# Optimization experiments

Measured on AMD Instinct MI355X. Metric: run time of the kernel, lower is better.

The kernel has to match this reference:

```python
import jax, jax.numpy as jnp
import numpy as np

TAU = 1.0
EPS = 1e-5


def _gcn_sparse(x, src, dst, ew, W, b, n):
    # PyG GCNConv: add self-loops (weight 1), sym-normalize, aggregate src->dst
    deg = jax.ops.segment_sum(ew, dst, num_segments=n) + 1.0
    dinv = jnp.where(deg > 0, jax.lax.rsqrt(deg), 0.0)
    h = x @ W
    coef = dinv[src] * ew * dinv[dst]              # [E]
    out = jax.ops.segment_sum(h[src] * coef[:, None], dst, num_segments=n)
    out = out + h * (dinv * dinv)[:, None]         # self-loop term
    return out + b


def _gcn_dense(x, A, W, b):
    # x: [B,N,d], A: [B,N,N] with A[b,i,j] = weight of edge j->i
    n = A.shape[-1]
    Ah = A + jnp.eye(n, dtype=A.dtype)
    deg = Ah.sum(-1)
    dinv = jnp.where(deg > 0, jax.lax.rsqrt(deg), 0.0)
    An = dinv[:, :, None] * Ah * dinv[:, None, :]
    return jnp.einsum('bij,bjd->bid', An, x @ W) + b


def _bn_silu(x, g, be, axes):
    # BatchNorm over node axis (training-mode batch stats, biased var) + SiLU
    m = x.mean(axes, keepdims=True)
    v = x.var(axes, keepdims=True)
    return jax.nn.silu(g * (x - m) * jax.lax.rsqrt(v + EPS) + be)


def setup_inputs() -> dict:
    key = jax.random.key(0)
    ks = jax.random.split(key, 12)
    B, NPG, EPER = 32, 1024, 16384
    CIN, C, K1, K2, OUT = 64, 128, 128, 32, 10
    N, E = B * NPG, B * EPER
    ei = jax.random.randint(ks[0], (2, E), 0, NPG, dtype=jnp.int32)
    off = jnp.repeat(jnp.arange(B, dtype=jnp.int32) * NPG, EPER)
    edge_index = ei + off[None, :]
    x = jax.random.normal(ks[1], (N, CIN), jnp.float32)
    batch = jnp.repeat(jnp.arange(B, dtype=jnp.int32), NPG)
    batch_ptr = jnp.arange(B + 1, dtype=jnp.int32) * NPG
    p = lambda k, s: jax.random.normal(k, s, jnp.float32) * 0.05
    return dict(
        x=x, edge_index=edge_index, batch=batch, batch_ptr=batch_ptr,
        w1a=p(ks[2], (CIN, C)), b1a=jnp.zeros((C,)), g1a=jnp.ones((C,)), be1a=jnp.zeros((C,)),
        w1b=p(ks[3], (C, C)), b1b=jnp.zeros((C,)), g1b=jnp.ones((C,)), be1b=jnp.zeros((C,)),
        wp1=p(ks[4], (C, K1)), bp1=jnp.zeros((K1,)),
        w2a=p(ks[5], (C, C)), b2a=jnp.zeros((C,)), g2a=jnp.ones((C,)), be2a=jnp.zeros((C,)),
        w2b=p(ks[6], (C, C)), b2b=jnp.zeros((C,)), g2b=jnp.ones((C,)), be2b=jnp.zeros((C,)),
        wp2=p(ks[7], (C, K2)), bp2=jnp.zeros((K2,)),
        wl=p(ks[8], (C, OUT)), bl=jnp.zeros((OUT,)))


def reference(x, edge_index, batch, batch_ptr,
              w1a, b1a, g1a, be1a, w1b, b1b, g1b, be1b, wp1, bp1,
              w2a, b2a, g2a, be2a, w2b, b2b, g2b, be2b, wp2, bp2,
              wl, bl):
    n = x.shape[0]
    B = batch_ptr.shape[0] - 1
    npg = n // B                                    # uniform nodes per graph
    src, dst = edge_index[0], edge_index[1]
    ew = jnp.ones((edge_index.shape[1],), x.dtype)  # edge_weight=None -> ones

    # ---- stack 1: sparse GCN residual blocks + stochastic pool ----
    h = _bn_silu(_gcn_sparse(x, src, dst, ew, w1a, b1a, n), g1a, be1a, 0)
    h = h + _bn_silu(_gcn_sparse(h, src, dst, ew, w1b, b1b, n), g1b, be1b, 0)
    s = jax.nn.softmax(_gcn_sparse(h, src, dst, ew, wp1, bp1, n) / TAU, -1)  # [n,K1]
    s3 = s.reshape(B, npg, -1)
    x2 = jnp.einsum('bnc,bnd->bcd', s3, h.reshape(B, npg, -1))   # s^T x  [B,K1,C]
    t = jax.ops.segment_sum(s[src] * ew[:, None], dst, num_segments=n)  # A s
    A2 = jnp.einsum('bnc,bnk->bck', s3, t.reshape(B, npg, -1))   # s^T A s [B,K1,K1]

    # ---- stack 2: dense GCN on pooled graph + stochastic pool ----
    h2 = _bn_silu(_gcn_dense(x2, A2, w2a, b2a), g2a, be2a, (0, 1))
    h2 = h2 + _bn_silu(_gcn_dense(h2, A2, w2b, b2b), g2b, be2b, (0, 1))
    s2 = jax.nn.softmax(_gcn_dense(h2, A2, wp2, bp2) / TAU, -1)  # [B,K1,K2]
    x3 = jnp.einsum('bnc,bnd->bcd', s2, h2)                      # [B,K2,C]

    # global mean pool over nodes per graph, linear, log_softmax
    g = x3.mean(axis=1)
    out = jax.nn.log_softmax(g @ wl + bl, axis=1)
    # aux losses are multiplied by 0 in the original forward -> exact zero
    return (out, jnp.zeros((), x.dtype))
```

## Files before the change

### kernel.cpp

```cpp
#include <hip/hip_runtime.h>
#include <cmath>

#define KSPLIT 8
#define ELL_ST 80

typedef __attribute__((ext_vector_type(8))) short short8;
typedef __attribute__((ext_vector_type(4))) float float4v;

static __device__ __forceinline__ unsigned short f2bf(float f){
  union { float f; unsigned u; } c; c.f = f;
  unsigned r = c.u + 0x7fff + ((c.u >> 16) & 1);
  return (unsigned short)(r >> 16);
}
static __device__ __forceinline__ float u2f(unsigned u){
  union { unsigned u; float f; } c; c.u = u; return c.f;
}
static __device__ __forceinline__ float silu(float y){ return y/(1.f+__expf(-y)); }

static __device__ __forceinline__ void coef_prologue(const float* __restrict__ stats,
                                                     const float* __restrict__ gamma,
                                                     const float* __restrict__ beta,
                                                     float invM, float* lds, int tbase){
  int t = threadIdx.x - tbase;
  if(t >= 0 && t < 128){
    float s = 0.f, q = 0.f;
    #pragma unroll
    for(int k=0;k<8;k++){ s += stats[k*128+t]; q += stats[1024 + k*128+t]; }
    float m = s*invM;
    float v = q*invM - m*m;
    float sc = gamma[t]*rsqrtf(v + 1e-5f);
    lds[t] = sc;
    lds[128+t] = beta[t] - m*sc;
  }
}

__global__ void k_fill_wt(const int* __restrict__ src, const int* __restrict__ dst,
                          int* __restrict__ cursor, int* __restrict__ esrc, int E,
                          const float* __restrict__ w1a, const float* __restrict__ w1b,
                          const float* __restrict__ wp1, unsigned short* __restrict__ t1a,
                          unsigned short* __restrict__ t1b, unsigned short* __restrict__ tp1,
                          int CIN){
  int i = blockIdx.x*256 + threadIdx.x;
  if(i < E){
    int d = dst[i];
    int p = atomicAdd(&cursor[d], 1);
    if(p < ELL_ST) esrc[(size_t)d*ELL_ST + p] = src[i];
  } else {
    int j = i - E;
    int n1 = CIN*128, n2 = 128*128;
    if(j >= 0 && j < n1){
      int k = j >> 7, c = j & 127;
      t1a[(size_t)c*CIN + k] = f2bf(w1a[j]);
    } else if(j >= n1 && j < n1+n2){
      int jj = j - n1; int k = jj >> 7, c = jj & 127;
      t1b[(size_t)c*128 + k] = f2bf(w1b[jj]);
    } else if(j >= n1+n2 && j < n1+2*n2){
      int jj = j - n1 - n2; int k = jj >> 7, c = jj & 127;
      tp1[(size_t)c*128 + k] = f2bf(wp1[jj]);
    }
  }
}

__global__ void k_gemm_mfma(const float* __restrict__ A, const float* __restrict__ A2,
                            const unsigned short* __restrict__ Bt,
                            unsigned short* __restrict__ Cb, int M, int K, int Nc,
                            const int* __restrict__ rowdeg,
                            const float* __restrict__ stA, const float* __restrict__ gA,
                            const float* __restrict__ beA,
                            const float* __restrict__ stB, const float* __restrict__ gB,
                            const float* __restrict__ beB, float invM){
  __shared__ unsigned short Abf[64][40];
  __shared__ unsigned short Bbf[64][40];
  __shared__ float lcA[256], lcB[256];
  int tid = threadIdx.x;
  if(stA) coef_prologue(stA, gA, beA, invM, lcA, 0);
  if(stB) coef_prologue(stB, gB, beB, invM, lcB, 128);
  if(stA || stB) __syncthreads();
  int wv = tid >> 6, lane = tid & 63;
  int quad = lane >> 4, l16 = lane & 15;
  int row0 = blockIdx.y*64, col0 = blockIdx.x*64;
  int sr = tid >> 2, sk = (tid & 3)*8;
  float4v acc[4] = {};
  for(int kt=0; kt<K; kt+=32){
    const float* ap = &A[(size_t)(row0+sr)*K + kt + sk];
    float va[8];
    *(float4*)&va[0] = *(const float4*)ap;
    *(float4*)&va[4] = *(const float4*)(ap+4);
    if(stB){
      const float* bp = &A2[(size_t)(row0+sr)*K + kt + sk];
      float vb[8];
      *(float4*)&vb[0] = *(const float4*)bp;
      *(float4*)&vb[4] = *(const float4*)(bp+4);
      #pragma unroll
      for(int i=0;i<8;i++){
        int c = kt+sk+i;
        va[i] = silu(lcA[c]*va[i] + lcA[128+c]) + silu(lcB[c]*vb[i] + lcB[128+c]);
      }
    } else if(stA){
      #pragma unroll
      for(int i=0;i<8;i++){
        int c = kt+sk+i;
        va[i] = silu(lcA[c]*va[i] + lcA[128+c]);
      }
    }
    uint4 pk;
    pk.x = (unsigned)f2bf(va[0]) | ((unsigned)f2bf(va[1])<<16);
    pk.y = (unsigned)f2bf(va[2]) | ((unsigned)f2bf(va[3])<<16);
    pk.z = (unsigned)f2bf(va[4]) | ((unsigned)f2bf(va[5])<<16);
    pk.w = (unsigned)f2bf(va[6]) | ((unsigned)f2bf(va[7])<<16);
    *(uint4*)&Abf[sr][sk] = pk;
    *(uint4*)&Bbf[sr][sk] = *(const uint4*)&Bt[(size_t)(col0+sr)*K + kt + sk];
    __syncthreads();
    short8 af = *(const short8*)&Abf[wv*16 + l16][quad*8];
    #pragma unroll
    for(int t=0;t<4;t++){
      short8 bf = *(const short8*)&Bbf[t*16 + l16][quad*8];
      acc[t] = __builtin_amdgcn_mfma_f32_16x16x32_bf16(af, bf, acc[t], 0, 0, 0);
    }
    __syncthreads();
  }
  float scr[4];
  #pragma unroll
  for(int r=0;r<4;r++){
    int grow = row0 + wv*16 + quad*4 + r;
    scr[r] = rowdeg ? rsqrtf((float)rowdeg[grow] + 1.0f) : 1.f;
  }
  #pragma unroll
  for(int t=0;t<4;t++){
    #pragma unroll
    for(int r=0;r<4;r++){
      int grow = row0 + wv*16 + quad*4 + r;
      int gcol = col0 + t*16 + l16;
      Cb[(size_t)grow*Nc + gcol] = f2bf(acc[t][r]*scr[r]);
    }
  }
}

__global__ void k_gemm64(const float* __restrict__ A, const float* __restrict__ B,
                         float* __restrict__ C, int M, int K, int Nc,
                         const float* __restrict__ rowscale,
                         const float* __restrict__ stA, const float* __restrict__ gA,
                         const float* __restrict__ beA, float invM){
  __shared__ float As[16][68];
  __shared__ float Bs[16][68];
  __shared__ float lc[256];
  int tid = threadIdx.x;
  if(stA){ coef_prologue(stA, gA, beA, invM, lc, 0); __syncthreads(); }
  int tx = tid & 15, ty = tid >> 4;
  int row0 = blockIdx.y*64, col0 = blockIdx.x*64;
  float acc[4][4] = {};
  for(int kt=0; kt<K; kt+=16){
    int ra = tid >> 2, ka = (tid & 3)*4;
    float4 va = *(const float4*)&A[(size_t)(row0+ra)*K + kt + ka];
    if(stA){
      float vv[4] = {va.x, va.y, va.z, va.w};
      #pragma unroll
      for(int i=0;i<4;i++){
        int c = kt+ka+i;
        vv[i] = silu(lc[c]*vv[i] + lc[128+c]);
      }
      va.x=vv[0]; va.y=vv[1]; va.z=vv[2]; va.w=vv[3];
    }
    As[ka+0][ra]=va.x; As[ka+1][ra]=va.y; As[ka+2][ra]=va.z; As[ka+3][ra]=va.w;
    int rb = tid >> 4, cb = (tid & 15)*4;
    *(float4*)&Bs[rb][cb] = *(const float4*)&B[(size_t)(kt+rb)*Nc + col0 + cb];
    __syncthreads();
    #pragma unroll
    for(int k=0;k<16;k++){
      float4 a = *(const float4*)&As[k][ty*4];
      float4 b = *(const float4*)&Bs[k][tx*4];
      float av[4]={a.x,a.y,a.z,a.w}, bv[4]={b.x,b.y,b.z,b.w};
      #pragma unroll
      for(int i=0;i<4;i++)
        #pragma unroll
        for(int j=0;j<4;j++) acc[i][j] += av[i]*bv[j];
    }
    __syncthreads();
  }
  #pragma unroll
  for(int i=0;i<4;i++){
    int r = row0 + ty*4 + i;
    float sc = rowscale ? rowscale[r] : 1.0f;
    float4 v; v.x=acc[i][0]*sc; v.y=acc[i][1]*sc; v.z=acc[i][2]*sc; v.w=acc[i][3]*sc;
    *(float4*)&C[(size_t)r*Nc + col0 + tx*4] = v;
  }
}

template<bool DO_SOFTMAX, bool GCN, bool STATS, bool BF16IN, bool BF16OUT>
__global__ void k_gather(const int* __restrict__ degc, const int* __restrict__ esrc,
                         const void* __restrict__ hWs,
                         const float* __restrict__ bias, float* __restrict__ out,
                         float* __restrict__ stats){
  __shared__ float lsum[4][128];
  __shared__ float lsq[4][128];
  const unsigned short* h16 = (const unsigned short*)hWs;
  const float* h32 = (const float*)hWs;
  int wave = threadIdx.x >> 6;
  int lane = threadIdx.x & 63;
  int bid = blockIdx.x;
  int d = ((bid & 7) << 12) | ((bid >> 3) << 2) | wave;
  int grp = lane >> 5;
  int c4 = (lane & 31)*4;
  int dgr = degc[d];
  int cnt = dgr > ELL_ST ? ELL_ST : dgr;
  cnt = __builtin_amdgcn_readfirstlane(cnt);
  const int* row = esrc + (size_t)d*ELL_ST;

  auto loadrow = [&](int s)->float4{
    if(BF16IN){
      uint2 u = *(const uint2*)&h16[(size_t)s*128 + c4];
      float4 v;
      v.x = u2f(u.x << 16); v.y = u2f(u.x & 0xffff0000u);
      v.z = u2f(u.y << 16); v.w = u2f(u.y & 0xffff0000u);
      return v;
    } else {
      return *(const float4*)&h32[(size_t)s*128 + c4];
    }
  };

  float4 a0 = {0.f,0.f,0.f,0.f}, a1 = {0.f,0.f,0.f,0.f};
  float4 a2 = {0.f,0.f,0.f,0.f}, a3 = {0.f,0.f,0.f,0.f};
  if(GCN && grp == 0)
    a0 = loadrow(d);
  for(int base=0; base<cnt; base+=32){
    int m = cnt - base; if(m > 32) m = 32;
    int idx = (lane < m) ? row[base + lane] : 0;
    int full = m & ~7;
    int j0 = 0;
    for(; j0 < full; j0 += 8){
      int s0 = __shfl(idx, j0+grp);
      int s1 = __shfl(idx, j0+grp+2);
      int s2 = __shfl(idx, j0+grp+4);
      int s3 = __shfl(idx, j0+grp+6);
      float4 v0 = loadrow(s0);
      float4 v1 = loadrow(s1);
      float4 v2 = loadrow(s2);
      float4 v3 = loadrow(s3);
      a0.x+=v0.x; a0.y+=v0.y; a0.z+=v0.z; a0.w+=v0.w;
      a1.x+=v1.x; a1.y+=v1.y; a1.z+=v1.z; a1.w+=v1.w;
      a2.x+=v2.x; a2.y+=v2.y; a2.z+=v2.z; a2.w+=v2.w;
      a3.x+=v3.x; a3.y+=v3.y; a3.z+=v3.z; a3.w+=v3.w;
    }
    if(j0 < m){
      int jj0 = j0+grp, jj1 = j0+grp+2, jj2 = j0+grp+4, jj3 = j0+grp+6;
      int s0 = __shfl(idx, jj0 < m ? jj0 : 0);
      int s1 = __shfl(idx, jj1 < m ? jj1 : 0);
      int s2 = __shfl(idx, jj2 < m ? jj2 : 0);
      int s3 = __shfl(idx, jj3 < m ? jj3 : 0);
      if(jj0 < m){ float4 v = loadrow(s0);
        a0.x+=v.x; a0.y+=v.y; a0.z+=v.z; a0.w+=v.w; }
      if(jj1 < m){ float4 v = loadrow(s1);
        a1.x+=v.x; a1.y+=v.y; a1.z+=v.z; a1.w+=v.w; }
      if(jj2 < m){ float4 v = loadrow(s2);
        a2.x+=v.x; a2.y+=v.y; a2.z+=v.z; a2.w+=v.w; }
      if(jj3 < m){ float4 v = loadrow(s3);
        a3.x+=v.x; a3.y+=v.y; a3.z+=v.z; a3.w+=v.w; }
    }
  }
  float4 acc;
  acc.x = (a0.x+a1.x)+(a2.x+a3.x);
  acc.y = (a0.y+a1.y)+(a2.y+a3.y);
  acc.z = (a0.z+a1.z)+(a2.z+a3.z);
  acc.w = (a0.w+a1.w)+(a2.w+a3.w);
  acc.x += __shfl_xor(acc.x, 32);
  acc.y += __shfl_xor(acc.y, 32);
  acc.z += __shfl_xor(acc.z, 32);
  acc.w += __shfl_xor(acc.w, 32);
  float4 val = acc;
  if(GCN){
    float dv = rsqrtf((float)dgr + 1.0f);
    float4 bi = *(const float4*)&bias[c4];
    val.x = dv*acc.x + bi.x; val.y = dv*acc.y + bi.y;
    val.z = dv*acc.z + bi.z; val.w = dv*acc.w + bi.w;
  }
  if(DO_SOFTMAX){
    float mx = fmaxf(fmaxf(val.x,val.y), fmaxf(val.z,val.w));
    #pragma unroll
    for(int o=1;o<32;o<<=1) mx = fmaxf(mx, __shfl_xor(mx,o));
    float4 e; e.x=__expf(val.x-mx); e.y=__expf(val.y-mx);
    e.z=__expf(val.z-mx); e.w=__expf(val.w-mx);
    float s = e.x+e.y+e.z+e.w;
    #pragma unroll
    for(int o=1;o<32;o<<=1) s += __shfl_xor(s,o);
    float inv = 1.f/s;
    val.x=e.x*inv; val.y=e.y*inv; val.z=e.z*inv; val.w=e.w*inv;
  }
  if(grp == 0){
    if(BF16OUT){
      unsigned short* o16 = (unsigned short*)out;
      uint2 w;
      w.x = (unsigned)f2bf(val.x) | ((unsigned)f2bf(val.y)<<16);
      w.y = (unsigned)f2bf(val.z) | ((unsigned)f2bf(val.w)<<16);
      *(uint2*)&o16[(size_t)d*128 + c4] = w;
    } else {
      *(float4*)&out[(size_t)d*128 + c4] = val;
    }
  }
  if(STATS){
    if(grp == 0){
      *(float4*)&lsum[wave][c4] = val;
      float4 q; q.x=val.x*val.x; q.y=val.y*val.y; q.z=val.z*val.z; q.w=val.w*val.w;
      *(float4*)&lsq[wave][c4] = q;
    }
    __syncthreads();
    int t = threadIdx.x;
    if(t < 128){
      float s = (lsum[0][t]+lsum[1][t]) + (lsum[2][t]+lsum[3][t]);
      atomicAdd(&stats[(bid & 7)*128 + t], s);
    } else {
      int c = t - 128;
      float q = (lsq[0][c]+lsq[1][c]) + (lsq[2][c]+lsq[3][c]);
      atomicAdd(&stats[1024 + (bid & 7)*128 + c], q);
    }
  }
}

__global__ __launch_bounds__(256, 2)
void k_pool2(const unsigned short* __restrict__ P, const float* __restrict__ Qa,
             const float* __restrict__ Qb, const unsigned short* __restrict__ Qc,
             const float* __restrict__ stA, const float* __restrict__ gA,
             const float* __restrict__ beA,
             const float* __restrict__ stB, const float* __restrict__ gB,
             const float* __restrict__ beB, float invM,
             float* __restrict__ part1, float* __restrict__ part2, int npg, int nb){
  __shared__ unsigned short sT[128][40];
  __shared__ unsigned short qT[128][40];
  __shared__ float lcA[256], lcB[256];
  int tid = threadIdx.x;
  bool fused = (blockIdx.z == 0);
  if(fused){
    coef_prologue(stA, gA, beA, invM, lcA, 0);
    coef_prologue(stB, gB, beB, invM, lcB, 128);
    __syncthreads();
  }
  int ks = blockIdx.x, b = blockIdx.y;
  int klen = npg / KSPLIT;
  size_t base = ((size_t)b*npg + (size_t)ks*klen)*128;
  int wv = tid >> 6, lane = tid & 63;
  int quad = lane >> 4, l16 = lane & 15;
  int wr = (wv >> 1)*64, wc = (wv & 1)*64;
  int arr = tid >> 7;
  int t7 = tid & 127;
  int sg = (t7 >> 4)*16;
  int sr2 = (t7 & 15)*2;
  float4v acc[4][4] = {};

  for(int c0 = 0; c0 < klen; c0 += 32){
    size_t i0 = base + (size_t)(c0+sr2)*128 + sg;
    if(arr == 0){
      uint4 ua = *(const uint4*)&P[i0];
      uint4 ub = *(const uint4*)&P[i0+8];
      uint4 uc = *(const uint4*)&P[i0+128];
      uint4 ud = *(const uint4*)&P[i0+136];
      unsigned short lo[16], hi[16];
      *(uint4*)&lo[0]=ua; *(uint4*)&lo[8]=ub;
      *(uint4*)&hi[0]=uc; *(uint4*)&hi[8]=ud;
      #pragma unroll
      for(int j=0;j<16;j++)
        *(unsigned*)&sT[sg+j][sr2] = (unsigned)lo[j] | ((unsigned)hi[j]<<16);
    } else if(fused){
      float va[16], vb[16], wa[16], wb[16];
      *(float4*)&va[0]  = *(const float4*)&Qa[i0];
      *(float4*)&va[4]  = *(const float4*)&Qa[i0+4];
      *(float4*)&va[8]  = *(const float4*)&Qa[i0+8];
      *(float4*)&va[12] = *(const float4*)&Qa[i0+12];
      *(float4*)&wa[0]  = *(const float4*)&Qa[i0+128];
      *(float4*)&wa[4]  = *(const float4*)&Qa[i0+132];
      *(float4*)&wa[8]  = *(const float4*)&Qa[i0+136];
      *(float4*)&wa[12] = *(const float4*)&Qa[i0+140];
      *(float4*)&vb[0]  = *(const float4*)&Qb[i0];
      *(float4*)&vb[4]  = *(const float4*)&Qb[i0+4];
      *(float4*)&vb[8]  = *(const float4*)&Qb[i0+8];
      *(float4*)&vb[12] = *(const float4*)&Qb[i0+12];
      *(float4*)&wb[0]  = *(const float4*)&Qb[i0+128];
      *(float4*)&wb[4]  = *(const float4*)&Qb[i0+132];
      *(float4*)&wb[8]  = *(const float4*)&Qb[i0+136];
      *(float4*)&wb[12] = *(const float4*)&Qb[i0+140];
      #pragma unroll
      for(int j=0;j<16;j++){
        int c = sg + j;
        float lo = silu(lcA[c]*va[j]+lcA[128+c]) + silu(lcB[c]*vb[j]+lcB[128+c]);
        float hi = silu(lcA[c]*wa[j]+lcA[128+c]) + silu(lcB[c]*wb[j]+lcB[128+c]);
        *(unsigned*)&qT[c][sr2] = (unsigned)f2bf(lo) | ((unsigned)f2bf(hi)<<16);
      }
    } else {
      uint4 ua = *(const uint4*)&Qc[i0];
      uint4 ub = *(const uint4*)&Qc[i0+8];
      uint4 uc = *(const uint4*)&Qc[i0+128];
      uint4 ud = *(const uint4*)&Qc[i0+136];
      unsigned short lo[16], hi[16];
      *(uint4*)&lo[0]=ua; *(uint4*)&lo[8]=ub;
      *(uint4*)&hi[0]=uc; *(uint4*)&hi[8]=ud;
      #pragma unroll
      for(int j=0;j<16;j++)
        *(unsigned*)&qT[sg+j][sr2] = (unsigned)lo[j] | ((unsigned)hi[j]<<16);
    }
    __syncthreads();
    #pragma unroll
    for(int i=0;i<4;i++){
      short8 af = *(const short8*)&sT[wr + i*16 + l16][quad*8];
      #pragma unroll
      for(int j=0;j<4;j++){
        short8 bf = *(const short8*)&qT[wc + j*16 + l16][quad*8];
        acc[i][j] = __builtin_amdgcn_mfma_f32_16x16x32_bf16(af, bf, acc[i][j], 0, 0, 0);
      }
    }
    __syncthreads();
  }

  float* outp = (fused ? part1 : part2) + ((size_t)(ks*nb + b)*128)*128;
  #pragma unroll
  for(int i=0;i<4;i++)
    #pragma unroll
    for(int r=0;r<4;r++){
      int m = wr + i*16 + quad*4 + r;
      #pragma unroll
      for(int j=0;j<4;j++)
        outp[(size_t)m*128 + wc + j*16 + l16] = acc[i][j][r];
    }
}

__global__ void k_pool_reduce2(const float* __restrict__ p1, const float* __restrict__ p2,
                               float* __restrict__ x2, float* __restrict__ A2,
                               float* __restrict__ dinv2, int total){
  int i = blockIdx.x*256 + threadIdx.x;
  int half = total >> 2;
  if(i < half){
    float4 s = *(const float4*)&p1[(size_t)i*4];
    #pragma unroll
    for(int ks=1; ks<KSPLIT; ks++){
      float4 v = *(const float4*)&p1[(size_t)ks*total + (size_t)i*4];
      s.x+=v.x; s.y+=v.y; s.z+=v.z; s.w+=v.w;
    }
    *(float4*)&x2[(size_t)i*4] = s;
  } else {
    int ia = i - half;
    float4 s = *(const float4*)&p2[(size_t)ia*4];
    #pragma unroll
    for(int ks=1; ks<KSPLIT; ks++){
      float4 v = *(const float4*)&p2[(size_t)ks*total + (size_t)ia*4];
      s.x+=v.x; s.y+=v.y; s.z+=v.z; s.w+=v.w;
    }
    *(float4*)&A2[(size_t)ia*4] = s;
    float rs = s.x+s.y+s.z+s.w;
    #pragma unroll
    for(int o=16;o>0;o>>=1) rs += __shfl_xor(rs, o);
    if((threadIdx.x & 31) == 0) dinv2[ia>>5] = rsqrtf(rs + 1.0f);
  }
}

__global__ void k_bgemm_post_stats(const float* __restrict__ A, const float* __restrict__ X,
                                   const float* __restrict__ dinv2, const float* __restrict__ bias,
                                   float* __restrict__ outp, float* __restrict__ stats){
  __shared__ float As[16][17], Xs[16][17];
  __shared__ float rs[16][17], rq[16][17];
  int b = blockIdx.z;
  int i0 = blockIdx.y*16, j0 = blockIdx.x*16;
  int tx = threadIdx.x, ty = threadIdx.y;
  const float* Ab = A + (size_t)b*16384;
  const float* Xb = X + (size_t)b*16384;
  float acc = 0.f;
  for(int k0=0;k0<128;k0+=16){
    As[ty][tx] = Ab[(i0+ty)*128 + k0+tx];
    Xs[ty][tx] = Xb[(k0+ty)*128 + j0+tx];
    __syncthreads();
    #pragma unroll
    for(int k=0;k<16;k++) acc += As[ty][k]*Xs[k][tx];
    __syncthreads();
  }
  int gr = b*128 + i0 + ty;
  float v = dinv2[gr]*(acc + Xb[(i0+ty)*128 + j0+tx]) + bias[j0+tx];
  outp[(size_t)gr*128 + j0+tx] = v;
  rs[ty][tx] = v; rq[ty][tx] = v*v;
  __syncthreads();
  if(ty == 0){
    float s = 0.f, q = 0.f;
    #pragma unroll
    for(int k=0;k<16;k++){ s += rs[k][tx]; q += rq[k][tx]; }
    int slot = b & 7;
    atomicAdd(&stats[slot*128 + j0+tx], s);
    atomicAdd(&stats[1024 + slot*128 + j0+tx], q);
  }
}

__global__ void k_final(const float* __restrict__ dTa, const float* __restrict__ dTb,
                        const float* __restrict__ stA, const float* __restrict__ gA,
                        const float* __restrict__ beA,
                        const float* __restrict__ stB, const float* __restrict__ gB,
                        const float* __restrict__ beB, float invMc,
                        const float* __restrict__ wl, const float* __restrict__ bl,
                        float* __restrict__ out, int K1n, int Cc, float inv_k2,
                        int OUTc, int zero_idx){
  __shared__ float lcA[256], lcB[256];
  __shared__ float red[256];
  __shared__ float gsh[128];
  __shared__ float logits[32];
  __shared__ float mred, lred;
  coef_prologue(stA, gA, beA, invMc, lcA, 0);
  coef_prologue(stB, gB, beB, invMc, lcB, 128);
  __syncthreads();
  int b = blockIdx.x;
  int tid = threadIdx.x;
  int c = tid & 127, rh = tid >> 7;
  const float* pa = dTa + (size_t)b*K1n*Cc;
  const float* pb = dTb + (size_t)b*K1n*Cc;
  float sa = lcA[c], ha = lcA[128+c], sb = lcB[c], hb = lcB[128+c];
  float acc = 0.f;
  for(int r = rh; r < K1n; r += 2){
    float ya = sa*pa[(size_t)r*Cc + c] + ha;
    float yb = sb*pb[(size_t)r*Cc + c] + hb;
    acc += silu(ya) + silu(yb);
  }
  red[tid] = acc;
  __syncthreads();
  if(tid < 128) gsh[tid] = (red[tid] + red[tid+128]) * inv_k2;
  __syncthreads();
  if(tid < OUTc){
    float l = bl[tid];
    for(int d=0; d<Cc; d++) l += gsh[d]*wl[d*OUTc + tid];
    logits[tid] = l;
  }
  __syncthreads();
  if(tid==0){
    float m = -1e30f;
    for(int o=0;o<OUTc;o++) m = fmaxf(m, logits[o]);
    float s = 0.f;
    for(int o=0;o<OUTc;o++) s += __expf(logits[o]-m);
    mred = m; lred = logf(s);
  }
  __syncthreads();
  if(tid < OUTc) out[b*OUTc + tid] = logits[tid] - mred - lred;
  if(b==0 && tid==0 && zero_idx >= 0) out[zero_idx] = 0.f;
}

extern "C" void kernel_launch(void* const* d_in, const int* in_sizes, int n_in,
                              void* d_out, int out_size, void* d_ws, size_t ws_size,
                              hipStream_t stream){
  const float* x    = (const float*)d_in[0];
  const int*   ei   = (const int*)d_in[1];
  const float* w1a  = (const float*)d_in[4];
  const float* b1a  = (const float*)d_in[5];
  const float* g1a  = (const float*)d_in[6];
  const float* be1a = (const float*)d_in[7];
  const float* w1b  = (const float*)d_in[8];
  const float* b1b  = (const float*)d_in[9];
  const float* g1b  = (const float*)d_in[10];
  const float* be1b = (const float*)d_in[11];
  const float* wp1  = (const float*)d_in[12];
  const float* bp1  = (const float*)d_in[13];
  const float* w2a  = (const float*)d_in[14];
  const float* b2a  = (const float*)d_in[15];
  const float* g2a  = (const float*)d_in[16];
  const float* be2a = (const float*)d_in[17];
  const float* w2b  = (const float*)d_in[18];
  const float* b2b  = (const float*)d_in[19];
  const float* g2b  = (const float*)d_in[20];
  const float* be2b = (const float*)d_in[21];
  const float* wl   = (const float*)d_in[24];
  const float* bl   = (const float*)d_in[25];
  float* out = (float*)d_out;

  const int C_   = in_sizes[5];
  const int CIN_ = in_sizes[4]/C_;
  const int N    = in_sizes[0]/CIN_;
  const int E    = in_sizes[1]/2;
  const int B_   = in_sizes[3]-1;
  const int NPG_ = N/B_;
  const int K1_  = in_sizes[13];
  const int K2_  = in_sizes[23];
  const int OUTc = in_sizes[25];
  const int M2   = B_*K1_;
  const int total = M2*C_;

  const int* srcI = ei;
  const int* dstI = ei + E;

  float* ws = (float*)d_ws;
  size_t o = 0;
  unsigned short* bufW = (unsigned short*)(ws + o); o += (size_t)N*C_/2;
  float* bufA  = ws + o; o += (size_t)N*C_;
  float* bufB  = ws + o; o += (size_t)N*C_;
  unsigned short* bufS = (unsigned short*)(ws + o); o += (size_t)N*C_/2;
  unsigned short* bufT = (unsigned short*)(ws + o); o += (size_t)N*C_/2;
  float* x2    = ws + o; o += (size_t)total;
  float* A2    = ws + o; o += (size_t)total;
  float* dinv2 = ws + o; o += (size_t)M2;
  float* st1a  = ws + o; o += 2048;
  float* st1b  = ws + o; o += 2048;
  float* stDa  = ws + o; o += 2048;
  float* stDb  = ws + o; o += 2048;
  int* cursor  = (int*)(ws + o); o += (size_t)N;
  float* part  = ws + o; o += (size_t)KSPLIT*total;
  float* part2 = ws + o; o += (size_t)KSPLIT*total;
  float* dW  = part;
  float* dTa = part + (size_t)total;
  float* dTb = part + 2*(size_t)total;
  unsigned short* wt1a = (unsigned short*)(ws + o); o += (size_t)CIN_*C_/2 + 64;
  unsigned short* wt1b = (unsigned short*)(ws + o); o += (size_t)C_*C_/2 + 64;
  unsigned short* wtp1 = (unsigned short*)(ws + o); o += (size_t)C_*C_/2 + 64;
  int* esrc    = (int*)(ws + o); o += (size_t)N*ELL_ST;
  (void)ws_size; (void)n_in;

  dim3 blk256(256);
  dim3 gblk(16,16);
  auto g1 = [](int n){ return dim3((unsigned)((n+255)/256)); };
  const float invN = 1.0f/N, invM2 = 1.0f/M2;

  hipMemsetAsync(st1a, 0, (size_t)4*2048*sizeof(float) + (size_t)N*sizeof(int), stream);
  k_fill_wt<<<g1(E + CIN_*C_ + 2*C_*C_), blk256, 0, stream>>>(srcI, dstI, cursor, esrc, E,
      w1a, w1b, wp1, wt1a, wt1b, wtp1, CIN_);

  dim3 gath((unsigned)(N/4));

  k_gemm_mfma<<<dim3(C_/64, N/64), blk256, 0, stream>>>(x, nullptr, wt1a, bufW, N, CIN_, C_, cursor,
      nullptr, nullptr, nullptr, nullptr, nullptr, nullptr, 0.f);
  k_gather<false,true,true,true,false><<<gath, blk256, 0, stream>>>(cursor, esrc, bufW, b1a, bufA, st1a);

  k_gemm_mfma<<<dim3(C_/64, N/64), blk256, 0, stream>>>(bufA, nullptr, wt1b, bufW, N, C_, C_, cursor,
      st1a, g1a, be1a, nullptr, nullptr, nullptr, invN);
  k_gather<false,true,true,true,false><<<gath, blk256, 0, stream>>>(cursor, esrc, bufW, b1b, bufB, st1b);

  k_gemm_mfma<<<dim3(K1_/64, N/64), blk256, 0, stream>>>(bufA, bufB, wtp1, bufW, N, C_, K1_, cursor,
      st1a, g1a, be1a, st1b, g1b, be1b, invN);
  k_gather<true,true,false,true,true><<<gath, blk256, 0, stream>>>(cursor, esrc, bufW, bp1, (float*)bufS, nullptr);
  k_gather<false,false,false,true,true><<<gath, blk256, 0, stream>>>(cursor, esrc, bufS, nullptr, (float*)bufT, nullptr);

  k_pool2<<<dim3(KSPLIT, B_, 2), blk256, 0, stream>>>(bufS, bufA, bufB, bufT,
      st1a, g1a, be1a, st1b, g1b, be1b, invN, part, part2, NPG_, B_);
  k_pool_reduce2<<<g1(total/2), blk256, 0, stream>>>(part, part2, x2, A2, dinv2, total);

  k_gemm64<<<dim3(C_/64, M2/64), blk256, 0, stream>>>(x2, w2a, dW, M2, C_, C_, dinv2,
      nullptr, nullptr, nullptr, 0.f);
  k_bgemm_post_stats<<<dim3(C_/16, K1_/16, B_), gblk, 0, stream>>>(A2, dW, dinv2, b2a, dTa, stDa);

  k_gemm64<<<dim3(C_/64, M2/64), blk256, 0, stream>>>(dTa, w2b, dW, M2, C_, C_, dinv2,
      stDa, g2a, be2a, invM2);
  k_bgemm_post_stats<<<dim3(C_/16, K1_/16, B_), gblk, 0, stream>>>(A2, dW, dinv2, b2b, dTb, stDb);

  int zero_idx = (out_size > B_*OUTc) ? B_*OUTc : -1;
  k_final<<<dim3((unsigned)B_), blk256, 0, stream>>>(dTa, dTb,
      stDa, g2a, be2a, stDb, g2b, be2b, invM2, wl, bl, out, K1_, C_, 1.0f/K2_,
      OUTc, zero_idx);
}
```

Before: 370.0 us.

## Widen MFMA GEMM to full 128 columns and export bf16 h for pooling

The node GEMM now computes all 128 output columns per block, so each A tile, along with its BN+SiLU prologue, is loaded and transformed once instead of twice. The third GEMM also writes the BN/SiLU-combined residual activation h as bf16 into a new buffer. The pooling kernel then reads that precomputed bf16 h instead of re-reading two fp32 buffers and recomputing normalization. This trades larger LDS and register use per block, plus an extra bf16 write, for less global traffic and duplicated elementwise work. It hardcodes the output width to 128.

```diff
diff --git a/kernel.cpp b/kernel.cpp
--- a/kernel.cpp
+++ b/kernel.cpp
@@ -63,14 +63,15 @@
 
 __global__ void k_gemm_mfma(const float* __restrict__ A, const float* __restrict__ A2,
                             const unsigned short* __restrict__ Bt,
-                            unsigned short* __restrict__ Cb, int M, int K, int Nc,
+                            unsigned short* __restrict__ Cb,
+                            unsigned short* __restrict__ Hout, int M, int K,
                             const int* __restrict__ rowdeg,
                             const float* __restrict__ stA, const float* __restrict__ gA,
                             const float* __restrict__ beA,
                             const float* __restrict__ stB, const float* __restrict__ gB,
                             const float* __restrict__ beB, float invM){
   __shared__ unsigned short Abf[64][40];
-  __shared__ unsigned short Bbf[64][40];
+  __shared__ unsigned short Bbf[128][40];
   __shared__ float lcA[256], lcB[256];
   int tid = threadIdx.x;
   if(stA) coef_prologue(stA, gA, beA, invM, lcA, 0);
@@ -78,9 +79,10 @@
   if(stA || stB) __syncthreads();
   int wv = tid >> 6, lane = tid & 63;
   int quad = lane >> 4, l16 = lane & 15;
-  int row0 = blockIdx.y*64, col0 = blockIdx.x*64;
+  int row0 = blockIdx.x*64;
   int sr = tid >> 2, sk = (tid & 3)*8;
-  float4v acc[4] = {};
+  int srb = tid >> 1, skb = (tid & 1)*16;
+  float4v acc[8] = {};
   for(int kt=0; kt<K; kt+=32){
     const float* ap = &A[(size_t)(row0+sr)*K + kt + sk];
     float va[8];
@@ -109,11 +111,14 @@
     pk.z = (unsigned)f2bf(va[4]) | ((unsigned)f2bf(va[5])<<16);
     pk.w = (unsigned)f2bf(va[6]) | ((unsigned)f2bf(va[7])<<16);
     *(uint4*)&Abf[sr][sk] = pk;
-    *(uint4*)&Bbf[sr][sk] = *(const uint4*)&Bt[(size_t)(col0+sr)*K + kt + sk];
+    if(Hout)
+      *(uint4*)&Hout[(size_t)(row0+sr)*128 + kt + sk] = pk;
+    *(uint4*)&Bbf[srb][skb]   = *(const uint4*)&Bt[(size_t)srb*K + kt + skb];
+    *(uint4*)&Bbf[srb][skb+8] = *(const uint4*)&Bt[(size_t)srb*K + kt + skb + 8];
     __syncthreads();
     short8 af = *(const short8*)&Abf[wv*16 + l16][quad*8];
     #pragma unroll
-    for(int t=0;t<4;t++){
+    for(int t=0;t<8;t++){
       short8 bf = *(const short8*)&Bbf[t*16 + l16][quad*8];
       acc[t] = __builtin_amdgcn_mfma_f32_16x16x32_bf16(af, bf, acc[t], 0, 0, 0);
     }
@@ -126,12 +131,11 @@
     scr[r] = rowdeg ? rsqrtf((float)rowdeg[grow] + 1.0f) : 1.f;
   }
   #pragma unroll
-  for(int t=0;t<4;t++){
+  for(int t=0;t<8;t++){
     #pragma unroll
     for(int r=0;r<4;r++){
       int grow = row0 + wv*16 + quad*4 + r;
-      int gcol = col0 + t*16 + l16;
-      Cb[(size_t)grow*Nc + gcol] = f2bf(acc[t][r]*scr[r]);
+      Cb[(size_t)grow*128 + t*16 + l16] = f2bf(acc[t][r]*scr[r]);
     }
   }
 }
@@ -316,23 +320,14 @@
 }
 
 __global__ __launch_bounds__(256, 2)
-void k_pool2(const unsigned short* __restrict__ P, const float* __restrict__ Qa,
-             const float* __restrict__ Qb, const unsigned short* __restrict__ Qc,
-             const float* __restrict__ stA, const float* __restrict__ gA,
-             const float* __restrict__ beA,
-             const float* __restrict__ stB, const float* __restrict__ gB,
-             const float* __restrict__ beB, float invM,
+void k_pool2(const unsigned short* __restrict__ P, const unsigned short* __restrict__ QH,
+             const unsigned short* __restrict__ QT,
              float* __restrict__ part1, float* __restrict__ part2, int npg, int nb){
   __shared__ unsigned short sT[128][40];
   __shared__ unsigned short qT[128][40];
-  __shared__ float lcA[256], lcB[256];
   int tid = threadIdx.x;
-  bool fused = (blockIdx.z == 0);
-  if(fused){
-    coef_prologue(stA, gA, beA, invM, lcA, 0);
-    coef_prologue(stB, gB, beB, invM, lcB, 128);
-    __syncthreads();
-  }
+  bool zq = (blockIdx.z == 0);
+  const unsigned short* Q = zq ? QH : QT;
   int ks = blockIdx.x, b = blockIdx.y;
   int klen = npg / KSPLIT;
   size_t base = ((size_t)b*npg + (size_t)ks*klen)*128;
@@ -347,54 +342,18 @@
 
   for(int c0 = 0; c0 < klen; c0 += 32){
     size_t i0 = base + (size_t)(c0+sr2)*128 + sg;
-    if(arr == 0){
-      uint4 ua = *(const uint4*)&P[i0];
-      uint4 ub = *(const uint4*)&P[i0+8];
-      uint4 uc = *(const uint4*)&P[i0+128];
-      uint4 ud = *(const uint4*)&P[i0+136];
-      unsigned short lo[16], hi[16];
-      *(uint4*)&lo[0]=ua; *(uint4*)&lo[8]=ub;
-      *(uint4*)&hi[0]=uc; *(uint4*)&hi[8]=ud;
-      #pragma unroll
-      for(int j=0;j<16;j++)
-        *(unsigned*)&sT[sg+j][sr2] = (unsigned)lo[j] | ((unsigned)hi[j]<<16);
-    } else if(fused){
-      float va[16], vb[16], wa[16], wb[16];
-      *(float4*)&va[0]  = *(const float4*)&Qa[i0];
-      *(float4*)&va[4]  = *(const float4*)&Qa[i0+4];
-      *(float4*)&va[8]  = *(const float4*)&Qa[i0+8];
-      *(float4*)&va[12] = *(const float4*)&Qa[i0+12];
-      *(float4*)&wa[0]  = *(const float4*)&Qa[i0+128];
-      *(float4*)&wa[4]  = *(const float4*)&Qa[i0+132];
-      *(float4*)&wa[8]  = *(const float4*)&Qa[i0+136];
-      *(float4*)&wa[12] = *(const float4*)&Qa[i0+140];
-      *(float4*)&vb[0]  = *(const float4*)&Qb[i0];
-      *(float4*)&vb[4]  = *(const float4*)&Qb[i0+4];
-      *(float4*)&vb[8]  = *(const float4*)&Qb[i0+8];
-      *(float4*)&vb[12] = *(const float4*)&Qb[i0+12];
-      *(float4*)&wb[0]  = *(const float4*)&Qb[i0+128];
-      *(float4*)&wb[4]  = *(const float4*)&Qb[i0+132];
-      *(float4*)&wb[8]  = *(const float4*)&Qb[i0+136];
-      *(float4*)&wb[12] = *(const float4*)&Qb[i0+140];
-      #pragma unroll
-      for(int j=0;j<16;j++){
-        int c = sg + j;
-        float lo = silu(lcA[c]*va[j]+lcA[128+c]) + silu(lcB[c]*vb[j]+lcB[128+c]);
-        float hi = silu(lcA[c]*wa[j]+lcA[128+c]) + silu(lcB[c]*wb[j]+lcB[128+c]);
-        *(unsigned*)&qT[c][sr2] = (unsigned)f2bf(lo) | ((unsigned)f2bf(hi)<<16);
-      }
-    } else {
-      uint4 ua = *(const uint4*)&Qc[i0];
-      uint4 ub = *(const uint4*)&Qc[i0+8];
-      uint4 uc = *(const uint4*)&Qc[i0+128];
-      uint4 ud = *(const uint4*)&Qc[i0+136];
-      unsigned short lo[16], hi[16];
-      *(uint4*)&lo[0]=ua; *(uint4*)&lo[8]=ub;
-      *(uint4*)&hi[0]=uc; *(uint4*)&hi[8]=ud;
-      #pragma unroll
-      for(int j=0;j<16;j++)
-        *(unsigned*)&qT[sg+j][sr2] = (unsigned)lo[j] | ((unsigned)hi[j]<<16);
-    }
+    const unsigned short* Sp = arr ? Q : P;
+    unsigned short (*dstT)[40] = arr ? qT : sT;
+    uint4 ua = *(const uint4*)&Sp[i0];
+    uint4 ub = *(const uint4*)&Sp[i0+8];
+    uint4 uc = *(const uint4*)&Sp[i0+128];
+    uint4 ud = *(const uint4*)&Sp[i0+136];
+    unsigned short lo[16], hi[16];
+    *(uint4*)&lo[0]=ua; *(uint4*)&lo[8]=ub;
+    *(uint4*)&hi[0]=uc; *(uint4*)&hi[8]=ud;
+    #pragma unroll
+    for(int j=0;j<16;j++)
+      *(unsigned*)&dstT[sg+j][sr2] = (unsigned)lo[j] | ((unsigned)hi[j]<<16);
     __syncthreads();
     #pragma unroll
     for(int i=0;i<4;i++){
@@ -408,7 +367,7 @@
     __syncthreads();
   }
 
-  float* outp = (fused ? part1 : part2) + ((size_t)(ks*nb + b)*128)*128;
+  float* outp = (zq ? part1 : part2) + ((size_t)(ks*nb + b)*128)*128;
   #pragma unroll
   for(int i=0;i<4;i++)
     #pragma unroll
@@ -582,6 +541,7 @@
   float* bufB  = ws + o; o += (size_t)N*C_;
   unsigned short* bufS = (unsigned short*)(ws + o); o += (size_t)N*C_/2;
   unsigned short* bufT = (unsigned short*)(ws + o); o += (size_t)N*C_/2;
+  unsigned short* bufH = (unsigned short*)(ws + o); o += (size_t)N*C_/2;
   float* x2    = ws + o; o += (size_t)total;
   float* A2    = ws + o; o += (size_t)total;
   float* dinv2 = ws + o; o += (size_t)M2;
@@ -611,22 +571,23 @@
       w1a, w1b, wp1, wt1a, wt1b, wtp1, CIN_);
 
   dim3 gath((unsigned)(N/4));
-
-  k_gemm_mfma<<<dim3(C_/64, N/64), blk256, 0, stream>>>(x, nullptr, wt1a, bufW, N, CIN_, C_, cursor,
+  dim3 gmm((unsigned)(N/64));
+
+  k_gemm_mfma<<<gmm, blk256, 0, stream>>>(x, nullptr, wt1a, bufW, nullptr, N, CIN_, cursor,
       nullptr, nullptr, nullptr, nullptr, nullptr, nullptr, 0.f);
   k_gather<false,true,true,true,false><<<gath, blk256, 0, stream>>>(cursor, esrc, bufW, b1a, bufA, st1a);
 
-  k_gemm_mfma<<<dim3(C_/64, N/64), blk256, 0, stream>>>(bufA, nullptr, wt1b, bufW, N, C_, C_, cursor,
+  k_gemm_mfma<<<gmm, blk256, 0, stream>>>(bufA, nullptr, wt1b, bufW, nullptr, N, C_, cursor,
       st1a, g1a, be1a, nullptr, nullptr, nullptr, invN);
   k_gather<false,true,true,true,false><<<gath, blk256, 0, stream>>>(cursor, esrc, bufW, b1b, bufB, st1b);
 
-  k_gemm_mfma<<<dim3(K1_/64, N/64), blk256, 0, stream>>>(bufA, bufB, wtp1, bufW, N, C_, K1_, cursor,
+  k_gemm_mfma<<<gmm, blk256, 0, stream>>>(bufA, bufB, wtp1, bufW, bufH, N, C_, cursor,
       st1a, g1a, be1a, st1b, g1b, be1b, invN);
   k_gather<true,true,false,true,true><<<gath, blk256, 0, stream>>>(cursor, esrc, bufW, bp1, (float*)bufS, nullptr);
   k_gather<false,false,false,true,true><<<gath, blk256, 0, stream>>>(cursor, esrc, bufS, nullptr, (float*)bufT, nullptr);
 
-  k_pool2<<<dim3(KSPLIT, B_, 2), blk256, 0, stream>>>(bufS, bufA, bufB, bufT,
-      st1a, g1a, be1a, st1b, g1b, be1b, invN, part, part2, NPG_, B_);
+  k_pool2<<<dim3(KSPLIT, B_, 2), blk256, 0, stream>>>(bufS, bufH, bufT,
+      part, part2, NPG_, B_);
   k_pool_reduce2<<<g1(total/2), blk256, 0, stream>>>(part, part2, x2, A2, dinv2, total);
 
   k_gemm64<<<dim3(C_/64, M2/64), blk256, 0, stream>>>(x2, w2a, dW, M2, C_, C_, dinv2,
```

After: 357.9 us. 3.3% less time.
